# Kernel optimization log

Hardware: AMD Instinct MI355X
Metric: run time of the kernel (lower is better)

The kernel has to match this reference:

```python
import jax, jax.numpy as jnp
import numpy as np

NP, NC, E, EL = 50000, 5000, 200000, 100000
DP, DC, HID, OUT, HEADS = 1280, 256, 128, 128, 4


def setup_inputs() -> dict:
    key = jax.random.key(0)
    ks = jax.random.split(key, 40)
    p = lambda k, shp: jax.random.normal(k, shp, dtype=jnp.float32) * 0.05
    inp = {
        "x_protein": jax.random.normal(ks[0], (NP, DP), dtype=jnp.float32),
        "x_class": jax.random.normal(ks[1], (NC, DC), dtype=jnp.float32),
        "src": jax.random.randint(ks[2], (E,), 0, NP),
        "dst": jax.random.randint(ks[3], (E,), 0, NC),
        "edge_label_src": jax.random.randint(ks[4], (EL,), 0, NP),
        "edge_label_dst": jax.random.randint(ks[5], (EL,), 0, NC),
        # SAGEConv, relation protein->class (updates class nodes)
        "sage_pc_Wl": p(ks[6], (DP, HID)), "sage_pc_bl": p(ks[7], (HID,)), "sage_pc_Wr": p(ks[8], (DC, HID)),
        # SAGEConv, relation class->protein (updates protein nodes)
        "sage_cp_Wl": p(ks[9], (DC, HID)), "sage_cp_bl": p(ks[10], (HID,)), "sage_cp_Wr": p(ks[11], (DP, HID)),
        # GATConv p->c (inputs are hidden after conv1)
        "gat_pc_Wsrc": p(ks[12], (HID, HEADS * HID)), "gat_pc_Wdst": p(ks[13], (HID, HEADS * HID)),
        "gat_pc_asrc": p(ks[14], (HEADS, HID)), "gat_pc_adst": p(ks[15], (HEADS, HID)), "gat_pc_b": p(ks[16], (HID,)),
        # GATConv c->p
        "gat_cp_Wsrc": p(ks[17], (HID, HEADS * HID)), "gat_cp_Wdst": p(ks[18], (HID, HEADS * HID)),
        "gat_cp_asrc": p(ks[19], (HEADS, HID)), "gat_cp_adst": p(ks[20], (HEADS, HID)), "gat_cp_b": p(ks[21], (HID,)),
        # final per-node-type Linear (to_hetero duplicates lin per node type)
        "lin_p_W": p(ks[22], (HID, OUT)), "lin_p_b": p(ks[23], (OUT,)),
        "lin_c_W": p(ks[24], (HID, OUT)), "lin_c_b": p(ks[25], (OUT,)),
        # link predictor
        "link_W": p(ks[26], (2 * OUT, 1)), "link_b": p(ks[27], (1,)),
    }
    return inp


def _sage(x_src, x_dst, s, d, Wl, bl, Wr, n_dst):
    # PyG SAGEConv: lin_l(mean_aggr(x_src)) + lin_r(x_dst); lin_l has bias.
    agg = jax.ops.segment_sum(x_src[s], d, num_segments=n_dst)
    cnt = jax.ops.segment_sum(jnp.ones((s.shape[0], 1), x_src.dtype), d, num_segments=n_dst)
    mean = agg / jnp.maximum(cnt, 1.0)
    return mean @ Wl + bl + x_dst @ Wr


def _gat(x_src, x_dst, s, d, Ws, Wd, a_s, a_d, b, n_dst):
    # PyG GATConv bipartite, heads=HEADS, concat=False, add_self_loops=False.
    H, C = a_s.shape
    hs = (x_src @ Ws).reshape(-1, H, C)   # [Ns, H, C]
    hd = (x_dst @ Wd).reshape(-1, H, C)   # [Nd, H, C]
    als = jnp.einsum('nhc,hc->nh', hs, a_s)
    ald = jnp.einsum('nhc,hc->nh', hd, a_d)
    e = jax.nn.leaky_relu(als[s] + ald[d], 0.2)                    # [E, H]
    emax = jax.ops.segment_max(e, d, num_segments=n_dst)          # stable softmax per dst
    ee = jnp.exp(e - emax[d])
    denom = jax.ops.segment_sum(ee, d, num_segments=n_dst)
    alpha = ee / denom[d]                                          # [E, H]
    out = jax.ops.segment_sum(alpha[:, :, None] * hs[s], d, num_segments=n_dst)  # [Nd, H, C]
    return out.mean(axis=1) + b  # concat=False -> mean over heads


def reference(x_protein, x_class, src, dst, edge_label_src, edge_label_dst,
              sage_pc_Wl, sage_pc_bl, sage_pc_Wr,
              sage_cp_Wl, sage_cp_bl, sage_cp_Wr,
              gat_pc_Wsrc, gat_pc_Wdst, gat_pc_asrc, gat_pc_adst, gat_pc_b,
              gat_cp_Wsrc, gat_cp_Wdst, gat_cp_asrc, gat_cp_adst, gat_cp_b,
              lin_p_W, lin_p_b, lin_c_W, lin_c_b, link_W, link_b):
    # Layer 1: hetero SAGE (each node type has exactly one incoming relation)
    h_c = jax.nn.relu(_sage(x_protein, x_class, src, dst, sage_pc_Wl, sage_pc_bl, sage_pc_Wr, NC))
    h_p = jax.nn.relu(_sage(x_class, x_protein, dst, src, sage_cp_Wl, sage_cp_bl, sage_cp_Wr, NP))
    # Layer 2: hetero GAT
    g_c = jax.nn.relu(_gat(h_p, h_c, src, dst, gat_pc_Wsrc, gat_pc_Wdst, gat_pc_asrc, gat_pc_adst, gat_pc_b, NC))
    g_p = jax.nn.relu(_gat(h_c, h_p, dst, src, gat_cp_Wsrc, gat_cp_Wdst, gat_cp_asrc, gat_cp_adst, gat_cp_b, NP))
    # Per-type output projection
    z_p = g_p @ lin_p_W + lin_p_b
    z_c = g_c @ lin_c_W + lin_c_b
    # Link predictor: gather, concat, linear, sigmoid
    ef = jnp.concatenate([z_p[edge_label_src], z_c[edge_label_dst]], axis=-1)  # [EL, 2*OUT]
    return jax.nn.sigmoid(ef @ link_W + link_b).squeeze(-1)
```

## Files before the change

kernel.cpp:

```cpp
#include <hip/hip_runtime.h>
#include <math.h>

#define NPROT 50000
#define NCLS  5000
#define DIMP  1280
#define DIMC  256
#define SCAN_N (NCLS + NPROT)
#define KSTEPS (DIMP/32)

#define P1B  ((NPROT+127)/128)
#define C1BY ((NCLS+63)/64)
#define C1B  (4*C1BY)

typedef float4 f4;
typedef __attribute__((ext_vector_type(8))) short short8;
typedef __attribute__((ext_vector_type(4))) float f32x4;

__device__ __forceinline__ unsigned short f2bf(float f){
    unsigned u = __float_as_uint(f);
    u += 0x7FFFu + ((u >> 16) & 1u);
    return (unsigned short)(u >> 16);
}
__device__ __forceinline__ float bf2f(unsigned short b){
    return __uint_as_float(((unsigned)b) << 16);
}
__device__ __forceinline__ void gload_lds16(const void* g, void* l){
    __builtin_amdgcn_global_load_lds((const __attribute__((address_space(1))) void*)g,
                                     (__attribute__((address_space(3))) void*)l, 16, 0, 0);
}
__device__ __forceinline__ int OFFV(const int* __restrict__ offv, const int* __restrict__ part, int v){
    return offv[v] + part[v>>10];
}

__global__ __launch_bounds__(512) void mega1(const float* __restrict__ Af,
                                             const unsigned short* __restrict__ BtP,
                                             unsigned short* __restrict__ P1,
                                             const float* __restrict__ Ac,
                                             const float* __restrict__ WcatC,
                                             unsigned short* __restrict__ C1,
                                             const int* __restrict__ src, const int* __restrict__ dst,
                                             const int* __restrict__ offv, const int* __restrict__ part,
                                             int* __restrict__ cur, int* __restrict__ adj, int E){
    __shared__ __align__(16) unsigned char smem[48*1024];
    const int blk = blockIdx.x;
    const int tid = threadIdx.x;

    if(blk < P1B){
        unsigned char* As = smem;
        unsigned char* Bs = smem + 16*1024;
        const int lane = tid & 63;
        const int w    = tid >> 6;
        const int wm   = w >> 2, wn = w & 3;
        const int row0 = blk * 128;
        const int kg = lane >> 4, fr = lane & 15;

        const int ar_  = tid >> 2;
        const int acc_ = tid & 3;
        const int asrow = min(row0 + ar_, NPROT-1);
        const float* aG = Af + (size_t)asrow*DIMP + acc_*8;
        const int awoff = ar_*64 + ((acc_ ^ ((ar_>>1)&3)) << 4);

        f32x4 acc[4][4] = {};
        f4 va, vb;

        auto STAGEB = [&](int buf, int k0){
            #pragma unroll
            for(int i=0;i<2;i++){
                int c  = i*512 + tid;
                int r  = c >> 2, cc = c & 3;
                int scc = cc ^ ((r>>1) & 3);
                gload_lds16((const void*)(BtP + (size_t)r*DIMP + k0 + scc*8),
                            (void*)(Bs + buf*16384 + (i*512 + w*64 + lane)*16));
            }
        };
        auto WRITEA = [&](int buf){
            union { short8 s; unsigned short u[8]; } uu;
            uu.u[0]=f2bf(va.x); uu.u[1]=f2bf(va.y); uu.u[2]=f2bf(va.z); uu.u[3]=f2bf(va.w);
            uu.u[4]=f2bf(vb.x); uu.u[5]=f2bf(vb.y); uu.u[6]=f2bf(vb.z); uu.u[7]=f2bf(vb.w);
            *(short8*)(As + buf*8192 + awoff) = uu.s;
        };

        va = *(const f4*)(aG + 0);
        vb = *(const f4*)(aG + 4);
        STAGEB(0, 0);
        WRITEA(0);
        __syncthreads();

        for(int t=0; t<KSTEPS; ++t){
            const int cb = t & 1;
            if(t+1 < KSTEPS){
                va = *(const f4*)(aG + (t+1)*32);
                vb = *(const f4*)(aG + (t+1)*32 + 4);
                STAGEB(cb^1, (t+1)*32);
            }

            short8 aF[4], bF[4];
            #pragma unroll
            for(int m=0;m<4;m++){
                int r = wm*64 + m*16 + fr;
                aF[m] = *(const short8*)(As + cb*8192 + r*64 + ((kg ^ ((r>>1)&3))<<4));
            }
            #pragma unroll
            for(int n=0;n<4;n++){
                int r = wn*64 + n*16 + fr;
                bF[n] = *(const short8*)(Bs + cb*16384 + r*64 + ((kg ^ ((r>>1)&3))<<4));
            }
            #pragma unroll
            for(int m=0;m<4;m++)
            #pragma unroll
            for(int n=0;n<4;n++)
                acc[m][n] = __builtin_amdgcn_mfma_f32_16x16x32_bf16(aF[m], bF[n], acc[m][n], 0, 0, 0);

            if(t+1 < KSTEPS) WRITEA(cb^1);
            __syncthreads();
        }

        #pragma unroll
        for(int m=0;m<4;m++)
        #pragma unroll
        for(int r=0;r<4;r++){
            int row = row0 + wm*64 + m*16 + kg*4 + r;
            if(row < NPROT){
                #pragma unroll
                for(int n=0;n<4;n++)
                    P1[(size_t)row*256 + wn*64 + n*16 + fr] = f2bf(acc[m][n][r]);
            }
        }
    } else if(blk < P1B + C1B){
        float (*As)[68] = (float(*)[68])smem;
        float (*Bs)[64] = (float(*)[64])(smem + 16*68*4);
        const int bi = blk - P1B;
        const int row0 = (bi >> 2) * 64;
        const int col0 = (bi & 3) * 64;
        const bool act = tid < 256;
        const int ty = tid >> 4;
        const int tx = tid & 15;
        const int m  = tid >> 2;
        const int kq = (tid & 3) << 2;
        const int kb = tid >> 4;
        const int c4 = (tid & 15) << 2;

        float acc[4][4];
        #pragma unroll
        for(int i=0;i<4;i++)
        #pragma unroll
            for(int j=0;j<4;j++) acc[i][j]=0.f;

        const bool arow_ok = act && (row0 + m) < NCLS;
        const float* Abase = Ac + (size_t)(row0 + min(m,255)) * DIMC + kq;
        const float* Bbase = WcatC + col0 + c4 + (size_t)kb * 256;

        for(int k0 = 0; k0 < DIMC; k0 += 16){
            if(act){
                f4 av;
                if(arow_ok) av = *(const f4*)(Abase + k0);
                else        av = make_float4(0.f,0.f,0.f,0.f);
                As[kq+0][m]=av.x; As[kq+1][m]=av.y; As[kq+2][m]=av.z; As[kq+3][m]=av.w;
                *(f4*)&Bs[kb][c4] = *(const f4*)(Bbase + (size_t)k0 * 256);
            }
            __syncthreads();
            if(act){
                #pragma unroll
                for(int kk=0;kk<16;kk++){
                    f4 a = *(const f4*)&As[kk][ty<<2];
                    f4 b = *(const f4*)&Bs[kk][tx<<2];
                    float ar[4]={a.x,a.y,a.z,a.w};
                    float br[4]={b.x,b.y,b.z,b.w};
                    #pragma unroll
                    for(int i=0;i<4;i++)
                    #pragma unroll
                        for(int j=0;j<4;j++) acc[i][j] += ar[i]*br[j];
                }
            }
            __syncthreads();
        }
        if(act){
            #pragma unroll
            for(int i=0;i<4;i++){
                int r = row0 + (ty<<2) + i;
                if(r < NCLS){
                    ushort4 v;
                    v.x=f2bf(acc[i][0]); v.y=f2bf(acc[i][1]);
                    v.z=f2bf(acc[i][2]); v.w=f2bf(acc[i][3]);
                    *(ushort4*)&C1[(size_t)r*256 + col0 + (tx<<2)] = v;
                }
            }
        }
    } else {
        int e = (blk - P1B - C1B)*512 + tid;
        if(e < E){
            int s = src[e], d = dst[e];
            int pc = atomicAdd(&cur[d],1);        adj[OFFV(offv,part,d)+pc] = s;
            int pp = atomicAdd(&cur[NCLS+s],1);   adj[OFFV(offv,part,NCLS+s)+pp] = d;
        }
    }
}

#define NPB ((NPROT+127)/128)
#define NCB ((NCLS+127)/128)
__global__ __launch_bounds__(256) void gemm_hs(const unsigned short* __restrict__ Ap,
                                               const unsigned short* __restrict__ Ac,
                                               const unsigned short* __restrict__ Btp,
                                               const unsigned short* __restrict__ Btc,
                                               const float* __restrict__ projP,
                                               const float* __restrict__ projC,
                                               unsigned short* __restrict__ Cp,
                                               unsigned short* __restrict__ Cc,
                                               float* __restrict__ attP,
                                               float* __restrict__ attC){
    const bool cls = (int)blockIdx.y >= NPB;
    const unsigned short* A  = cls ? Ac : Ap;
    const unsigned short* Bt = cls ? Btc : Btp;
    unsigned short* C = cls ? Cc : Cp;
    const int M = cls ? NCLS : NPROT;
    const int row0 = (cls ? blockIdx.y - NPB : blockIdx.y) * 128;
    const int col0 = blockIdx.x * 128;

    __shared__ __align__(16) unsigned char As[128*32*2];
    __shared__ __align__(16) unsigned char Bs[128*32*2];
    __shared__ float projS[1024];
    const int tid  = threadIdx.x;
    const int lane = tid & 63;
    const int w    = tid >> 6;
    const int wm   = w >> 1, wn = w & 1;
    const int kg = lane >> 4, fr = lane & 15;

    f32x4 acc[4][4] = {};

    for(int k0 = 0; k0 < 128; k0 += 32){
        #pragma unroll
        for(int i=0;i<2;i++){
            int c  = i*256 + w*64 + lane;
            int r  = c >> 2, cc = c & 3;
            int scc = cc ^ ((r>>1) & 3);
            int srow = min(row0 + r, M-1);
            gload_lds16((const void*)(A + (size_t)srow*128 + k0 + scc*8),
                        (void*)(As + (i*256 + w*64)*16));
        }
        #pragma unroll
        for(int i=0;i<2;i++){
            int c  = i*256 + w*64 + lane;
            int r  = c >> 2, cc = c & 3;
            int scc = cc ^ ((r>>1) & 3);
            gload_lds16((const void*)(Bt + (size_t)(col0 + r)*128 + k0 + scc*8),
                        (void*)(Bs + (i*256 + w*64)*16));
        }
        __syncthreads();

        short8 aF[4], bF[4];
        #pragma unroll
        for(int m=0;m<4;m++){
            int r = wm*64 + m*16 + fr;
            int b0 = (r*64 + kg*16) ^ (((r>>1)&3)<<4);
            aF[m] = *(const short8*)(As + b0);
        }
        #pragma unroll
        for(int n=0;n<4;n++){
            int r = wn*64 + n*16 + fr;
            int b0 = (r*64 + kg*16) ^ (((r>>1)&3)<<4);
            bF[n] = *(const short8*)(Bs + b0);
        }
        #pragma unroll
        for(int m=0;m<4;m++)
        #pragma unroll
        for(int n=0;n<4;n++)
            acc[m][n] = __builtin_amdgcn_mfma_f32_16x16x32_bf16(aF[m], bF[n], acc[m][n], 0, 0, 0);
        __syncthreads();
    }

    #pragma unroll
    for(int m=0;m<4;m++)
    #pragma unroll
    for(int r=0;r<4;r++){
        int row = row0 + wm*64 + m*16 + kg*4 + r;
        if(row < M){
            #pragma unroll
            for(int n=0;n<4;n++)
                C[(size_t)row*512 + col0 + wn*64 + n*16 + fr] = f2bf(acc[m][n][r]);
        }
    }

    if(blockIdx.x == 0){
        const float* proj = cls ? projC : projP;
        float* att = cls ? attC : attP;
        for(int i=tid;i<1024;i+=256) projS[i] = proj[i];
        __syncthreads();
        int ri = tid >> 1, cb = (tid & 1)*4;
        int row = row0 + ri;
        if(row < M){
            const unsigned short* ar = A + (size_t)row*128;
            float s0=0.f,s1=0.f,s2=0.f,s3=0.f;
            #pragma unroll
            for(int kk=0;kk<16;kk++){
                short8 a8 = *(const short8*)(ar + kk*8);
                #pragma unroll
                for(int q=0;q<8;q++){
                    float av = bf2f((unsigned short)a8[q]);
                    const float* pr = &projS[(kk*8+q)*8 + cb];
                    s0 += av*pr[0]; s1 += av*pr[1]; s2 += av*pr[2]; s3 += av*pr[3];
                }
            }
            f4 o = make_float4(s0,s1,s2,s3);
            *(f4*)&att[(size_t)row*8 + cb] = o;
        }
    }
}

__global__ void setup(const float* __restrict__ Wl_pc, const float* __restrict__ Wr_cp,
                      const float* __restrict__ Wl_cp, const float* __restrict__ Wr_pc,
                      const float* __restrict__ pcWs, const float* __restrict__ pcAs,
                      const float* __restrict__ pcWd, const float* __restrict__ pcAd,
                      const float* __restrict__ cpWs, const float* __restrict__ cpAs,
                      const float* __restrict__ cpWd, const float* __restrict__ cpAd,
                      const float* __restrict__ lpW, const float* __restrict__ lpb,
                      const float* __restrict__ lcW, const float* __restrict__ lcb,
                      const float* __restrict__ linkW,
                      const int* __restrict__ src, const int* __restrict__ dst,
                      unsigned short* __restrict__ BtP, float* __restrict__ WcatC,
                      unsigned short* __restrict__ BtSp, unsigned short* __restrict__ BtSc,
                      float* __restrict__ projP, float* __restrict__ projC,
                      float* __restrict__ w_p, float* __restrict__ w_c,
                      float* __restrict__ cpc,
                      int* __restrict__ deg, int E){
    int blk = blockIdx.x, tid = threadIdx.x;
    if(blk < 2048){
        int t = blk*256 + tid;
        if(t < 327680){
            int n = t / 1280, k = t % 1280;
            float v = (n<128) ? Wl_pc[(size_t)k*128+n] : Wr_cp[(size_t)k*128+n-128];
            BtP[t] = f2bf(v);
        } else if(t < 393216){
            int i = t - 327680; int k = i>>8, j = i&255;
            WcatC[i] = (j<128) ? Wl_cp[(size_t)k*128+j] : Wr_pc[(size_t)k*128+j-128];
        } else if(t < 458752){
            int i = t - 393216; int n = i>>7, k = i&127;
            BtSp[i] = f2bf(pcWs[(size_t)k*512+n]);
        } else {
            int i = t - 458752; int n = i>>7, k = i&127;
            BtSc[i] = f2bf(cpWs[(size_t)k*512+n]);
        }
    } else if(blk < 2056){
        int sec = (blk-2048) >> 1;
        int t = ((blk-2048) & 1)*256 + tid;
        const float *W, *a; float* proj; int colbase;
        if(sec==0){ W=pcWs; a=pcAs; proj=projP; colbase=0; }
        else if(sec==1){ W=cpWd; a=cpAd; proj=projP; colbase=4; }
        else if(sec==2){ W=pcWd; a=pcAd; proj=projC; colbase=0; }
        else { W=cpWs; a=cpAs; proj=projC; colbase=4; }
        int k = t >> 2, h = t & 3;
        const float* w = W + (size_t)k*512 + h*128;
        const float* av = a + h*128;
        float s=0.f;
        for(int c=0;c<128;c++) s += w[c]*av[c];
        proj[k*8 + colbase + h] = s;
    } else if(blk == 2056){
        if(tid < 128){
            float s=0.f;
            for(int o=0;o<128;o++) s += lpW[(size_t)tid*128+o]*linkW[o];
            w_p[tid]=s;
        } else {
            int j=tid-128;
            float s=0.f;
            for(int o=0;o<128;o++) s += lcW[(size_t)j*128+o]*linkW[128+o];
            w_c[j]=s;
        }
        if(tid==0){ float s=0.f; for(int o=0;o<128;o++) s+=lpb[o]*linkW[o];      cpc[0]=s; }
        if(tid==1){ float s=0.f; for(int o=0;o<128;o++) s+=lcb[o]*linkW[128+o];  cpc[1]=s; }
    } else {
        int e = (blk-2057)*256 + tid;
        if(e < E){
            atomicAdd(&deg[dst[e]],1);
            atomicAdd(&deg[NCLS + src[e]],1);
        }
    }
}

__global__ __launch_bounds__(1024) void scan1(const int* __restrict__ in, int* __restrict__ out,
                                              int* __restrict__ part, int n){
    __shared__ int buf[1024];
    int tid = threadIdx.x;
    int g = blockIdx.x*1024 + tid;
    int v = (g<n) ? in[g] : 0;
    buf[tid] = v;
    __syncthreads();
    for(int o=1;o<1024;o<<=1){
        int t = (tid>=o) ? buf[tid-o] : 0;
        __syncthreads();
        buf[tid] += t;
        __syncthreads();
    }
    if(g<n) out[g] = buf[tid] - v;
    if(tid==1023) part[blockIdx.x] = buf[1023];
}
__global__ __launch_bounds__(64) void scan2(int* __restrict__ part, int nb,
                                            int* __restrict__ offv, int n){
    int tid = threadIdx.x;
    int orig = (tid<nb) ? part[tid] : 0;
    int v = orig;
    #pragma unroll
    for(int o=1;o<64;o<<=1){
        int t = __shfl_up(v, o);
        if(tid>=o) v += t;
    }
    int total = __shfl(v, nb-1);
    if(tid<nb) part[tid] = v - orig;
    if(tid == (n>>10)) offv[n] = total - (v - orig);
}

__global__ __launch_bounds__(256) void sage_all(const int* __restrict__ offv, const int* __restrict__ part,
                                                const int* __restrict__ adj,
                                                const unsigned short* __restrict__ P1,
                                                const unsigned short* __restrict__ C1,
                                                const float* __restrict__ bl_pc, const float* __restrict__ bl_cp,
                                                unsigned short* __restrict__ h_c, unsigned short* __restrict__ h_p){
    int v = blockIdx.x*4 + (threadIdx.x>>6);
    int l = threadIdx.x & 63;
    if(v >= SCAN_N) return;
    int b = OFFV(offv,part,v), deg = OFFV(offv,part,v+1)-b;
    float a0=0.f, a1=0.f;
    float inv = 1.f/(float)max(deg,1);
    if(v < NCLS){
        for(int i=0;i<deg;i++){
            int s = adj[b+i];
            ushort2 w = *((const ushort2*)P1 + (size_t)s*128 + l);
            a0 += bf2f(w.x); a1 += bf2f(w.y);
        }
        ushort2 sv = *((const ushort2*)C1 + (size_t)v*128 + 64 + l);
        float h0 = fmaxf(a0*inv + bl_pc[2*l]   + bf2f(sv.x), 0.f);
        float h1 = fmaxf(a1*inv + bl_pc[2*l+1] + bf2f(sv.y), 0.f);
        ushort2 o; o.x=f2bf(h0); o.y=f2bf(h1);
        *((ushort2*)h_c + (size_t)v*64 + l) = o;
    } else {
        int m = v - NCLS;
        for(int i=0;i<deg;i++){
            int d = adj[b+i];
            ushort2 w = *((const ushort2*)C1 + (size_t)d*128 + l);
            a0 += bf2f(w.x); a1 += bf2f(w.y);
        }
        ushort2 sv = *((const ushort2*)P1 + (size_t)m*128 + 64 + l);
        float h0 = fmaxf(a0*inv + bl_cp[2*l]   + bf2f(sv.x), 0.f);
        float h1 = fmaxf(a1*inv + bl_cp[2*l+1] + bf2f(sv.y), 0.f);
        ushort2 o; o.x=f2bf(h0); o.y=f2bf(h1);
        *((ushort2*)h_p + (size_t)m*64 + l) = o;
    }
}

__global__ __launch_bounds__(128) void gat_all(const int* __restrict__ offv, const int* __restrict__ part,
                                               const int* __restrict__ adj,
                                               const float* __restrict__ attP, const float* __restrict__ attC,
                                               const unsigned short* __restrict__ hs_p,
                                               const unsigned short* __restrict__ hs_c,
                                               const float* __restrict__ gb_pc, const float* __restrict__ gb_cp,
                                               const float* __restrict__ w_c, const float* __restrict__ w_p,
                                               const float* __restrict__ cpc,
                                               float* __restrict__ u_c, float* __restrict__ u_p){
    __shared__ float ald[4];
    __shared__ int   adjS[32];
    __shared__ float eeS[32*4];
    __shared__ float den8[8];
    __shared__ f4    red4[32];

    int n = blockIdx.x;
    const bool cls = n < NCLS;
    const int node = cls ? n : n - NCLS;
    const float* attS = cls ? attP : attC;
    const float* attD = cls ? attC : attP;
    const int abase = cls ? 0 : 4;
    const unsigned short* hs = cls ? hs_p : hs_c;
    const float* gb = cls ? gb_pc : gb_cp;
    const float* wv = cls ? w_c : w_p;
    float* u = cls ? u_c : u_p;
    const int cidx = cls ? 1 : 0;

    int j = threadIdx.x;
    const int hh = j >> 5;
    const int q  = j & 31;
    int b = OFFV(offv,part,n), deg = OFFV(offv,part,n+1)-b;
    if(j < 4) ald[j] = attD[(size_t)node*8 + abase + j];

    float a0=0.f, a1=0.f, a2=0.f, a3=0.f;
    float denP = 0.f;

    for(int base=0; base<deg; base+=32){
        int cnt = min(32, deg-base);
        if(j < cnt) adjS[j] = adj[b+base+j];
        __syncthreads();
        if(j < cnt*4){
            int i = j>>2, h = j&3;
            int s = adjS[i];
            float e = attS[(size_t)s*8 + abase + h] + ald[h];
            e = e > 0.f ? e : 0.2f*e;
            float ee = __expf(e);
            eeS[j] = ee;
            denP += ee;
        }
        __syncthreads();
        for(int ii=0; ii<cnt; ii++){
            int s = adjS[ii];
            float ee = eeS[ii*4 + hh];
            ushort4 v = *(const ushort4*)(hs + (size_t)s*512 + hh*128 + q*4);
            a0 += ee*bf2f(v.x); a1 += ee*bf2f(v.y);
            a2 += ee*bf2f(v.z); a3 += ee*bf2f(v.w);
        }
        __syncthreads();
    }

    float dp = denP;
    dp += __shfl_xor(dp, 4);
    dp += __shfl_xor(dp, 8);
    dp += __shfl_xor(dp, 16);
    dp += __shfl_xor(dp, 32);
    if((j & 63) < 4) den8[(j>>6)*4 + (j&3)] = dp;
    __syncthreads();

    float den_h = den8[hh] + den8[4+hh];
    float inv = (deg > 0) ? 0.25f/den_h : 0.f;
    a0 *= inv; a1 *= inv; a2 *= inv; a3 *= inv;

    a0 += __shfl_xor(a0, 32); a1 += __shfl_xor(a1, 32);
    a2 += __shfl_xor(a2, 32); a3 += __shfl_xor(a3, 32);
    if(j >= 64 && j < 96) red4[q] = make_float4(a0,a1,a2,a3);
    __syncthreads();
    float val = 0.f;
    if(j < 32){
        f4 r = red4[q];
        float t0 = a0 + r.x, t1 = a1 + r.y, t2 = a2 + r.z, t3 = a3 + r.w;
        const float* gbq = gb + q*4;
        const float* wvq = wv + q*4;
        val = fmaxf(t0 + gbq[0], 0.f)*wvq[0]
            + fmaxf(t1 + gbq[1], 0.f)*wvq[1]
            + fmaxf(t2 + gbq[2], 0.f)*wvq[2]
            + fmaxf(t3 + gbq[3], 0.f)*wvq[3];
    }
    #pragma unroll
    for(int o=16;o;o>>=1) val += __shfl_down(val, o);
    if(j == 0) u[node] = val + cpc[cidx];
}

__global__ void link_out(const int* __restrict__ els, const int* __restrict__ eld,
                         const float* __restrict__ u_p, const float* __restrict__ u_c,
                         const float* __restrict__ linkb, float* __restrict__ out, int EL){
    int i = blockIdx.x*256 + threadIdx.x;
    if(i >= EL) return;
    float x = u_p[els[i]] + u_c[eld[i]] + linkb[0];
    out[i] = 1.f/(1.f + __expf(-x));
}

extern "C" void kernel_launch(void* const* d_in, const int* in_sizes, int n_in,
                              void* d_out, int out_size, void* d_ws, size_t ws_size,
                              hipStream_t stream){
    const float* x_p  = (const float*)d_in[0];
    const float* x_c  = (const float*)d_in[1];
    const int*   src  = (const int*)d_in[2];
    const int*   dst  = (const int*)d_in[3];
    const int*   els  = (const int*)d_in[4];
    const int*   eld  = (const int*)d_in[5];
    const float* sage_pc_Wl = (const float*)d_in[6];
    const float* sage_pc_bl = (const float*)d_in[7];
    const float* sage_pc_Wr = (const float*)d_in[8];
    const float* sage_cp_Wl = (const float*)d_in[9];
    const float* sage_cp_bl = (const float*)d_in[10];
    const float* sage_cp_Wr = (const float*)d_in[11];
    const float* gat_pc_Wsrc = (const float*)d_in[12];
    const float* gat_pc_Wdst = (const float*)d_in[13];
    const float* gat_pc_asrc = (const float*)d_in[14];
    const float* gat_pc_adst = (const float*)d_in[15];
    const float* gat_pc_b    = (const float*)d_in[16];
    const float* gat_cp_Wsrc = (const float*)d_in[17];
    const float* gat_cp_Wdst = (const float*)d_in[18];
    const float* gat_cp_asrc = (const float*)d_in[19];
    const float* gat_cp_adst = (const float*)d_in[20];
    const float* gat_cp_b    = (const float*)d_in[21];
    const float* lin_p_W = (const float*)d_in[22];
    const float* lin_p_b = (const float*)d_in[23];
    const float* lin_c_W = (const float*)d_in[24];
    const float* lin_c_b = (const float*)d_in[25];
    const float* link_W  = (const float*)d_in[26];
    const float* link_b  = (const float*)d_in[27];

    const int E  = in_sizes[2];
    const int EL = in_sizes[4];

    float* ws = (float*)d_ws;
    size_t off = 0;
    auto alloc = [&](size_t n)->float*{ float* p = ws + off; off += (n + 3) & ~(size_t)3; return p; };

    unsigned short* BtP  = (unsigned short*)alloc((size_t)256*DIMP/2);
    float* WcatC = alloc((size_t)DIMC*256);
    unsigned short* BtSp = (unsigned short*)alloc((size_t)512*128/2);
    unsigned short* BtSc = (unsigned short*)alloc((size_t)512*128/2);
    unsigned short* P1   = (unsigned short*)alloc((size_t)NPROT*256/2);
    unsigned short* C1   = (unsigned short*)alloc((size_t)NCLS*256/2);
    unsigned short* h_p  = (unsigned short*)alloc((size_t)NPROT*128/2);
    unsigned short* h_c  = (unsigned short*)alloc((size_t)NCLS*128/2);
    unsigned short* hs_p = (unsigned short*)alloc((size_t)NPROT*512/2);
    unsigned short* hs_c = (unsigned short*)alloc((size_t)NCLS*512/2);
    float* attP  = alloc((size_t)NPROT*8);
    float* attC  = alloc((size_t)NCLS*8);
    float* projP = alloc(128*8);
    float* projC = alloc(128*8);
    float* w_p   = alloc(128);
    float* w_c   = alloc(128);
    float* cpc   = alloc(4);
    int* degcur = (int*)alloc((size_t)2*SCAN_N);
    int* deg = degcur;
    int* cur = degcur + SCAN_N;
    int* offv = (int*)alloc(SCAN_N+1);
    int* part = (int*)alloc(64);
    int* adj  = (int*)alloc((size_t)2*E);
    float* u_p = alloc(NPROT);
    float* u_c = alloc(NCLS);
    if(off*4 > ws_size) return;

    hipMemsetAsync(degcur, 0, (size_t)2*SCAN_N*4, stream);

    setup<<<2057 + (E+255)/256, 256, 0, stream>>>(
        sage_pc_Wl, sage_cp_Wr, sage_cp_Wl, sage_pc_Wr,
        gat_pc_Wsrc, gat_pc_asrc, gat_pc_Wdst, gat_pc_adst,
        gat_cp_Wsrc, gat_cp_asrc, gat_cp_Wdst, gat_cp_adst,
        lin_p_W, lin_p_b, lin_c_W, lin_c_b, link_W,
        src, dst,
        BtP, WcatC, BtSp, BtSc, projP, projC, w_p, w_c, cpc, deg, E);

    const int NB = (SCAN_N + 1023)/1024;
    scan1<<<NB,1024,0,stream>>>(deg, offv, part, SCAN_N);
    scan2<<<1,64,0,stream>>>(part, NB, offv, SCAN_N);

    const int FILLB = (E+511)/512;
    mega1<<<P1B + C1B + FILLB, 512, 0, stream>>>(x_p, BtP, P1, x_c, WcatC, C1,
                                                 src, dst, offv, part, cur, adj, E);

    sage_all<<<(SCAN_N+3)/4,256,0,stream>>>(offv, part, adj, P1, C1, sage_pc_bl, sage_cp_bl, h_c, h_p);

    gemm_hs<<<dim3(4,NPB+NCB),256,0,stream>>>(h_p, h_c, BtSp, BtSc, projP, projC,
                                              hs_p, hs_c, attP, attC);

    gat_all<<<SCAN_N,128,0,stream>>>(offv, part, adj, attP, attC, hs_p, hs_c,
                                     gat_pc_b, gat_cp_b, w_c, w_p, cpc, u_c, u_p);

    link_out<<<(EL+255)/256,256,0,stream>>>(els, eld, u_p, u_c, link_b, (float*)d_out, EL);
}
```

Baseline: 298.6 us.

## Shrink mega1 GEMM tiles to 64 rows with 256-thread blocks and unroll gather loops

The fused mega1 kernel now uses 256-thread blocks. The protein GEMM tile shrinks from 128 to 64 rows, with each of the 4 waves owning a 64-column slice, and shared memory drops to 40KB with launch_bounds(256,4). The class GEMM and edge-fill parts are adapted to the smaller block, which removes their idle half-block. The aim is more resident blocks per CU and more blocks across the grid. The cost is that each B tile is reused by fewer A rows, so B traffic rises. Gather loops in sage_all and gat_all also get unroll-4 pragmas to expose more memory-level parallelism.

```diff
diff --git a/kernel.cpp b/kernel.cpp
--- a/kernel.cpp
+++ b/kernel.cpp
@@ -8,7 +8,7 @@
 #define SCAN_N (NCLS + NPROT)
 #define KSTEPS (DIMP/32)
 
-#define P1B  ((NPROT+127)/128)
+#define P1B  ((NPROT+63)/64)
 #define C1BY ((NCLS+63)/64)
 #define C1B  (4*C1BY)
 
@@ -32,26 +32,25 @@
     return offv[v] + part[v>>10];
 }
 
-__global__ __launch_bounds__(512) void mega1(const float* __restrict__ Af,
-                                             const unsigned short* __restrict__ BtP,
-                                             unsigned short* __restrict__ P1,
-                                             const float* __restrict__ Ac,
-                                             const float* __restrict__ WcatC,
-                                             unsigned short* __restrict__ C1,
-                                             const int* __restrict__ src, const int* __restrict__ dst,
-                                             const int* __restrict__ offv, const int* __restrict__ part,
-                                             int* __restrict__ cur, int* __restrict__ adj, int E){
-    __shared__ __align__(16) unsigned char smem[48*1024];
+__global__ __launch_bounds__(256,4) void mega1(const float* __restrict__ Af,
+                                               const unsigned short* __restrict__ BtP,
+                                               unsigned short* __restrict__ P1,
+                                               const float* __restrict__ Ac,
+                                               const float* __restrict__ WcatC,
+                                               unsigned short* __restrict__ C1,
+                                               const int* __restrict__ src, const int* __restrict__ dst,
+                                               const int* __restrict__ offv, const int* __restrict__ part,
+                                               int* __restrict__ cur, int* __restrict__ adj, int E){
+    __shared__ __align__(16) unsigned char smem[40*1024];
     const int blk = blockIdx.x;
     const int tid = threadIdx.x;
 
     if(blk < P1B){
         unsigned char* As = smem;
-        unsigned char* Bs = smem + 16*1024;
+        unsigned char* Bs = smem + 8*1024;
         const int lane = tid & 63;
         const int w    = tid >> 6;
-        const int wm   = w >> 2, wn = w & 3;
-        const int row0 = blk * 128;
+        const int row0 = blk * 64;
         const int kg = lane >> 4, fr = lane & 15;
 
         const int ar_  = tid >> 2;
@@ -65,19 +64,19 @@
 
         auto STAGEB = [&](int buf, int k0){
             #pragma unroll
-            for(int i=0;i<2;i++){
-                int c  = i*512 + tid;
+            for(int i=0;i<4;i++){
+                int c  = i*256 + tid;
                 int r  = c >> 2, cc = c & 3;
                 int scc = cc ^ ((r>>1) & 3);
                 gload_lds16((const void*)(BtP + (size_t)r*DIMP + k0 + scc*8),
-                            (void*)(Bs + buf*16384 + (i*512 + w*64 + lane)*16));
+                            (void*)(Bs + buf*16384 + (i*256 + tid)*16));
             }
         };
         auto WRITEA = [&](int buf){
             union { short8 s; unsigned short u[8]; } uu;
             uu.u[0]=f2bf(va.x); uu.u[1]=f2bf(va.y); uu.u[2]=f2bf(va.z); uu.u[3]=f2bf(va.w);
             uu.u[4]=f2bf(vb.x); uu.u[5]=f2bf(vb.y); uu.u[6]=f2bf(vb.z); uu.u[7]=f2bf(vb.w);
-            *(short8*)(As + buf*8192 + awoff) = uu.s;
+            *(short8*)(As + buf*4096 + awoff) = uu.s;
         };
 
         va = *(const f4*)(aG + 0);
@@ -94,16 +93,18 @@
                 STAGEB(cb^1, (t+1)*32);
             }
 
+            const unsigned char* Ab = As + cb*4096;
+            const unsigned char* Bb = Bs + cb*16384;
             short8 aF[4], bF[4];
             #pragma unroll
             for(int m=0;m<4;m++){
-                int r = wm*64 + m*16 + fr;
-                aF[m] = *(const short8*)(As + cb*8192 + r*64 + ((kg ^ ((r>>1)&3))<<4));
+                int r = m*16 + fr;
+                aF[m] = *(const short8*)(Ab + r*64 + ((kg ^ ((r>>1)&3))<<4));
             }
             #pragma unroll
             for(int n=0;n<4;n++){
-                int r = wn*64 + n*16 + fr;
-                bF[n] = *(const short8*)(Bs + cb*16384 + r*64 + ((kg ^ ((r>>1)&3))<<4));
+                int r = w*64 + n*16 + fr;
+                bF[n] = *(const short8*)(Bb + r*64 + ((kg ^ ((r>>1)&3))<<4));
             }
             #pragma unroll
             for(int m=0;m<4;m++)
@@ -119,20 +120,19 @@
         for(int m=0;m<4;m++)
         #pragma unroll
         for(int r=0;r<4;r++){
-            int row = row0 + wm*64 + m*16 + kg*4 + r;
+            int row = row0 + m*16 + kg*4 + r;
             if(row < NPROT){
                 #pragma unroll
                 for(int n=0;n<4;n++)
-                    P1[(size_t)row*256 + wn*64 + n*16 + fr] = f2bf(acc[m][n][r]);
+                    P1[(size_t)row*256 + w*64 + n*16 + fr] = f2bf(acc[m][n][r]);
             }
         }
     } else if(blk < P1B + C1B){
-        float (*As)[68] = (float(*)[68])smem;
-        float (*Bs)[64] = (float(*)[64])(smem + 16*68*4);
+        float (*As64)[68] = (float(*)[68])smem;
+        float (*Bs64)[64] = (float(*)[64])(smem + 16*68*4);
         const int bi = blk - P1B;
         const int row0 = (bi >> 2) * 64;
         const int col0 = (bi & 3) * 64;
-        const bool act = tid < 256;
         const int ty = tid >> 4;
         const int tx = tid & 15;
         const int m  = tid >> 2;
@@ -146,48 +146,42 @@
         #pragma unroll
             for(int j=0;j<4;j++) acc[i][j]=0.f;
 
-        const bool arow_ok = act && (row0 + m) < NCLS;
-        const float* Abase = Ac + (size_t)(row0 + min(m,255)) * DIMC + kq;
+        const bool arow_ok = (row0 + m) < NCLS;
+        const float* Abase = Ac + (size_t)(row0 + m) * DIMC + kq;
         const float* Bbase = WcatC + col0 + c4 + (size_t)kb * 256;
 
         for(int k0 = 0; k0 < DIMC; k0 += 16){
-            if(act){
-                f4 av;
-                if(arow_ok) av = *(const f4*)(Abase + k0);
-                else        av = make_float4(0.f,0.f,0.f,0.f);
-                As[kq+0][m]=av.x; As[kq+1][m]=av.y; As[kq+2][m]=av.z; As[kq+3][m]=av.w;
-                *(f4*)&Bs[kb][c4] = *(const f4*)(Bbase + (size_t)k0 * 256);
-            }
+            f4 av;
+            if(arow_ok) av = *(const f4*)(Abase + k0);
+            else        av = make_float4(0.f,0.f,0.f,0.f);
+            As64[kq+0][m]=av.x; As64[kq+1][m]=av.y; As64[kq+2][m]=av.z; As64[kq+3][m]=av.w;
+            *(f4*)&Bs64[kb][c4] = *(const f4*)(Bbase + (size_t)k0 * 256);
             __syncthreads();
-            if(act){
+            #pragma unroll
+            for(int kk=0;kk<16;kk++){
+                f4 a = *(const f4*)&As64[kk][ty<<2];
+                f4 b = *(const f4*)&Bs64[kk][tx<<2];
+                float ar[4]={a.x,a.y,a.z,a.w};
+                float br[4]={b.x,b.y,b.z,b.w};
                 #pragma unroll
-                for(int kk=0;kk<16;kk++){
-                    f4 a = *(const f4*)&As[kk][ty<<2];
-                    f4 b = *(const f4*)&Bs[kk][tx<<2];
-                    float ar[4]={a.x,a.y,a.z,a.w};
-                    float br[4]={b.x,b.y,b.z,b.w};
-                    #pragma unroll
-                    for(int i=0;i<4;i++)
-                    #pragma unroll
-                        for(int j=0;j<4;j++) acc[i][j] += ar[i]*br[j];
-                }
+                for(int i=0;i<4;i++)
+                #pragma unroll
+                    for(int j=0;j<4;j++) acc[i][j] += ar[i]*br[j];
             }
             __syncthreads();
         }
-        if(act){
-            #pragma unroll
-            for(int i=0;i<4;i++){
-                int r = row0 + (ty<<2) + i;
-                if(r < NCLS){
-                    ushort4 v;
-                    v.x=f2bf(acc[i][0]); v.y=f2bf(acc[i][1]);
-                    v.z=f2bf(acc[i][2]); v.w=f2bf(acc[i][3]);
-                    *(ushort4*)&C1[(size_t)r*256 + col0 + (tx<<2)] = v;
-                }
+        #pragma unroll
+        for(int i=0;i<4;i++){
+            int r = row0 + (ty<<2) + i;
+            if(r < NCLS){
+                ushort4 v;
+                v.x=f2bf(acc[i][0]); v.y=f2bf(acc[i][1]);
+                v.z=f2bf(acc[i][2]); v.w=f2bf(acc[i][3]);
+                *(ushort4*)&C1[(size_t)r*256 + col0 + (tx<<2)] = v;
             }
         }
     } else {
-        int e = (blk - P1B - C1B)*512 + tid;
+        int e = (blk - P1B - C1B)*256 + tid;
         if(e < E){
             int s = src[e], d = dst[e];
             int pc = atomicAdd(&cur[d],1);        adj[OFFV(offv,part,d)+pc] = s;
@@ -420,6 +414,7 @@
     float a0=0.f, a1=0.f;
     float inv = 1.f/(float)max(deg,1);
     if(v < NCLS){
+        #pragma unroll 4
         for(int i=0;i<deg;i++){
             int s = adj[b+i];
             ushort2 w = *((const ushort2*)P1 + (size_t)s*128 + l);
@@ -432,6 +427,7 @@
         *((ushort2*)h_c + (size_t)v*64 + l) = o;
     } else {
         int m = v - NCLS;
+        #pragma unroll 4
         for(int i=0;i<deg;i++){
             int d = adj[b+i];
             ushort2 w = *((const ushort2*)C1 + (size_t)d*128 + l);
@@ -495,6 +491,7 @@
             denP += ee;
         }
         __syncthreads();
+        #pragma unroll 4
         for(int ii=0; ii<cnt; ii++){
             int s = adjS[ii];
             float ee = eeS[ii*4 + hh];
@@ -626,8 +623,8 @@
     scan1<<<NB,1024,0,stream>>>(deg, offv, part, SCAN_N);
     scan2<<<1,64,0,stream>>>(part, NB, offv, SCAN_N);
 
-    const int FILLB = (E+511)/512;
-    mega1<<<P1B + C1B + FILLB, 512, 0, stream>>>(x_p, BtP, P1, x_c, WcatC, C1,
+    const int FILLB = (E+255)/256;
+    mega1<<<P1B + C1B + FILLB, 256, 0, stream>>>(x_p, BtP, P1, x_c, WcatC, C1,
                                                  src, dst, offv, part, cur, adj, E);
 
     sage_all<<<(SCAN_N+3)/4,256,0,stream>>>(offv, part, adj, P1, C1, sage_pc_bl, sage_cp_bl, h_c, h_p);
```

After: 307.4 us. 3.0% more time.
